# Kernel optimization log

Measured on AMD Instinct MI355X. Metric: run time of the kernel, lower is better.

The kernel has to match this reference:

```python
import jax, jax.numpy as jnp
import numpy as np

MAX_INT = 1e4  # sentinel used by the original (transitions into START / out of STOP forbidden)
VOCAB, E, H, T, B, S = 50257, 512, 1024, 50, 8, 512  # T = tagset_size + 2


def _lstm_scan(x, h0, c0, Wih, Whh, b):
    # x: [time, batch, E] (time axis is the ORIGINAL batch dim, faithful to the
    # torch code which feeds [B,S,E] into a batch_first=False LSTM)
    def step(carry, xt):
        h, c = carry
        g = xt @ Wih.T + h @ Whh.T + b
        i, f, gg, o = jnp.split(g, 4, axis=-1)  # torch gate order i,f,g,o
        c = jax.nn.sigmoid(f) * c + jax.nn.sigmoid(i) * jnp.tanh(gg)
        h = jax.nn.sigmoid(o) * jnp.tanh(c)
        return (h, c), h
    _, hs = jax.lax.scan(step, (h0, c0), x)
    return hs


def setup_inputs() -> dict:
    key = jax.random.key(0)
    k = jax.random.split(key, 14)
    Hd = H // 2
    X = jax.random.randint(k[0], (B, S), 0, VOCAB)
    Y = jax.random.randint(k[1], (B, S), 0, T - 2)  # real tags only (no start/stop)
    h0 = jax.random.normal(k[2], (2, S, Hd), jnp.float32)
    c0 = jax.random.normal(k[3], (2, S, Hd), jnp.float32)
    emb_table = jax.random.normal(k[4], (VOCAB, E), jnp.float32) * 0.02
    Wih_f = jax.random.normal(k[5], (4 * Hd, E), jnp.float32) * 0.05
    Whh_f = jax.random.normal(k[6], (4 * Hd, Hd), jnp.float32) * 0.05
    b_f = jnp.zeros((4 * Hd,), jnp.float32)
    Wih_b = jax.random.normal(k[7], (4 * Hd, E), jnp.float32) * 0.05
    Whh_b = jax.random.normal(k[8], (4 * Hd, Hd), jnp.float32) * 0.05
    b_b = jnp.zeros((4 * Hd,), jnp.float32)
    fc_W = jax.random.normal(k[9], (T, H), jnp.float32) * 0.05
    fc_b = jnp.zeros((T,), jnp.float32)
    tr = jax.random.normal(k[10], (T, T), jnp.float32)
    transitions = tr.at[-2, :].set(-MAX_INT).at[:, -1].set(-MAX_INT)
    return {"X": X, "Y": Y, "h0": h0, "c0": c0, "emb_table": emb_table,
            "Wih_f": Wih_f, "Whh_f": Whh_f, "b_f": b_f,
            "Wih_b": Wih_b, "Whh_b": Whh_b, "b_b": b_b,
            "fc_W": fc_W, "fc_b": fc_b, "transitions": transitions}


def reference(X, Y, h0, c0, emb_table, Wih_f, Whh_f, b_f, Wih_b, Whh_b, b_b, fc_W, fc_b, transitions):
    emb = emb_table[X]                                   # [B,S,E]
    # BiLSTM: torch sees axis0 as time (faithful quirk), hidden batch == S
    hf = _lstm_scan(emb, h0[0], c0[0], Wih_f, Whh_f, b_f)
    hb = _lstm_scan(emb[::-1], h0[1], c0[1], Wih_b, Whh_b, b_b)[::-1]
    lstm_out = jnp.concatenate([hf, hb], axis=-1)        # [B,S,H]
    feats = lstm_out @ fc_W.T + fc_b                     # [B,S,T]
    nB, Tt = X.shape[0], transitions.shape[0]
    # CRF forward algorithm (log partition), vectorized over tags
    init = jnp.full((nB, Tt), -MAX_INT, feats.dtype).at[:, -2].set(0.0)
    def crf_step(fv, feat):                              # fv [B,T], feat [B,T]
        nv = fv[:, None, :] + transitions[None, :, :] + feat[:, :, None]  # [B,next,prev]
        return jax.nn.logsumexp(nv, axis=2), None
    fv, _ = jax.lax.scan(crf_step, init, jnp.swapaxes(feats, 0, 1))
    forward_score = jax.nn.logsumexp(fv + transitions[-1][None, :], axis=1).sum()
    # gold path score
    start = jnp.full((nB, 1), Tt - 2, dtype=Y.dtype)
    tags = jnp.concatenate([start, Y], axis=1)           # [B,S+1]
    trans_sc = transitions[tags[:, 1:], tags[:, :-1]].sum()
    emit_sc = jnp.take_along_axis(feats, tags[:, 1:, None], axis=2)[..., 0].sum()
    gold_score = trans_sc + emit_sc + transitions[-1, tags[:, -1]].sum()
    score = forward_score - gold_score
    return score, Y
```

## Files before the change

kernel.cpp:

```cpp
#include <hip/hip_runtime.h>
#include <hip/hip_bf16.h>

typedef __attribute__((ext_vector_type(4))) float f32x4;
typedef __attribute__((ext_vector_type(8))) short short8;

#define LN2F 0.69314718055994531f

__device__ __forceinline__ unsigned short f2b(float x){
  union{float f;unsigned u;}v; v.f=x;
  unsigned r = v.u + 0x7fffu + ((v.u>>16)&1u);
  return (unsigned short)(r>>16);
}
__device__ __forceinline__ float b2f(unsigned short h){
  union{unsigned u;float f;}v; v.u = ((unsigned)h)<<16; return v.f;
}
__device__ __forceinline__ float sigm(float x){ return 1.f/(1.f+__expf(-x)); }
__device__ __forceinline__ float tanh_(float x){ float t=__expf(2.f*x); return 1.f - 2.f/(t+1.f); }

__device__ __forceinline__ void gll16(const void* g, void* l){
  __builtin_amdgcn_global_load_lds((const __attribute__((address_space(1))) void*)g,
                                   (__attribute__((address_space(3))) void*)l, 16, 0, 0);
}

__global__ __launch_bounds__(256) void prep_kernel(
  const int* __restrict__ X, const int* __restrict__ Y,
  const float* __restrict__ h0, const float* __restrict__ c0,
  const float* __restrict__ emb,
  const float* __restrict__ WihF, const float* __restrict__ WihB,
  const float* __restrict__ WhhFf, const float* __restrict__ WhhBf,
  const float* __restrict__ fcWf, const float* __restrict__ trans,
  unsigned short* __restrict__ Abf, unsigned short* __restrict__ Wcat,
  unsigned short* __restrict__ WhhF, unsigned short* __restrict__ WhhB,
  unsigned short* __restrict__ hbufs, float* __restrict__ cbuf,
  unsigned short* __restrict__ fcW, unsigned short* __restrict__ Ebf,
  float* __restrict__ out)
{
  const int tid = blockIdx.x*256 + threadIdx.x;
  const int nth = gridDim.x*256;
  for(int i=tid;i<524288;i+=nth){
    int r = i>>7, q = i&127;
    float4 v = ((const float4*)(emb + (size_t)X[r]*512))[q];
    ushort4 o; o.x=f2b(v.x); o.y=f2b(v.y); o.z=f2b(v.z); o.w=f2b(v.w);
    ((ushort4*)Abf)[i] = o;
  }
  for(int i=tid;i<524288;i+=nth){
    int r = i>>7, q = i&127;
    const float* src = (r<2048) ? (WihF + (size_t)r*512) : (WihB + (size_t)(r-2048)*512);
    float4 v = ((const float4*)src)[q];
    ushort4 o; o.x=f2b(v.x); o.y=f2b(v.y); o.z=f2b(v.z); o.w=f2b(v.w);
    ((ushort4*)Wcat)[i] = o;
  }
  for(int i=tid;i<262144;i+=nth){
    float4 v = ((const float4*)WhhFf)[i];
    ushort4 o; o.x=f2b(v.x); o.y=f2b(v.y); o.z=f2b(v.z); o.w=f2b(v.w);
    ((ushort4*)WhhF)[i] = o;
  }
  for(int i=tid;i<262144;i+=nth){
    float4 v = ((const float4*)WhhBf)[i];
    ushort4 o; o.x=f2b(v.x); o.y=f2b(v.y); o.z=f2b(v.z); o.w=f2b(v.w);
    ((ushort4*)WhhB)[i] = o;
  }
  for(int i=tid;i<131072;i+=nth){
    int d = i>>16, rest = i&65535;
    float4 v = ((const float4*)h0)[i];
    ushort4 o; o.x=f2b(v.x); o.y=f2b(v.y); o.z=f2b(v.z); o.w=f2b(v.w);
    ((ushort4*)hbufs)[(size_t)(d*2)*65536 + rest] = o;
  }
  for(int i=tid;i<131072;i+=nth) ((float4*)cbuf)[i] = ((const float4*)c0)[i];
  for(int i=tid;i<16384;i+=nth){
    int n = i>>8, q = i&255;
    float4 v;
    if (n<50) v = ((const float4*)(fcWf + (size_t)n*1024))[q];
    else { v.x=0.f; v.y=0.f; v.z=0.f; v.w=0.f; }
    ushort4 o; o.x=f2b(v.x); o.y=f2b(v.y); o.z=f2b(v.z); o.w=f2b(v.w);
    ((ushort4*)fcW)[i] = o;
  }
  for(int i=tid;i<4096;i+=nth){
    int n = i>>6, p = i&63;
    float v = (n<50 && p<50) ? __expf(trans[n*50+p]) : 0.f;
    Ebf[i] = f2b(v);
  }
  for(int i=tid;i<4096;i+=nth) out[1+i] = (float)Y[i];
}

__global__ __launch_bounds__(256) void gemm1_kernel(const unsigned short* __restrict__ A,
                                                    const unsigned short* __restrict__ B,
                                                    unsigned short* __restrict__ C){
  __shared__ __align__(16) unsigned short As[128*32];
  __shared__ __align__(16) unsigned short Bs[128*32];
  const int t = threadIdx.x, w = t>>6, l = t&63;
  const int m0 = blockIdx.x<<7, n0 = blockIdx.y<<7;
  const int wr = (w>>1)<<6, wc = (w&1)<<6;
  const int fr = l&15, fk = (l>>4)<<3;
  f32x4 acc[4][4];
  #pragma unroll
  for(int i=0;i<4;i++)
    #pragma unroll
    for(int j=0;j<4;j++) acc[i][j]=(f32x4)0.f;
  const unsigned short* Ab = A + (size_t)m0*512;
  const unsigned short* Bb = B + (size_t)n0*512;
  const int r0 = (w<<5) + (l>>2);
  const int c0 = (l&3)<<3;
  unsigned short* asd = As + (w<<5)*32;
  unsigned short* bsd = Bs + (w<<5)*32;
  for(int kt=0; kt<16; ++kt){
    __syncthreads();
    const int kc = (kt<<5) + c0;
    gll16(Ab + (size_t)r0*512 + kc,      asd);
    gll16(Ab + (size_t)(r0+16)*512 + kc, asd + 16*32);
    gll16(Bb + (size_t)r0*512 + kc,      bsd);
    gll16(Bb + (size_t)(r0+16)*512 + kc, bsd + 16*32);
    asm volatile("s_waitcnt vmcnt(0)" ::: "memory");
    __syncthreads();
    short8 af[4], bf[4];
    #pragma unroll
    for(int mi=0;mi<4;mi++) af[mi] = *(const short8*)&As[(wr+mi*16+fr)*32 + fk];
    #pragma unroll
    for(int ni=0;ni<4;ni++) bf[ni] = *(const short8*)&Bs[(wc+ni*16+fr)*32 + fk];
    #pragma unroll
    for(int mi=0;mi<4;mi++)
      #pragma unroll
      for(int ni=0;ni<4;ni++)
        acc[mi][ni] = __builtin_amdgcn_mfma_f32_16x16x32_bf16(af[mi], bf[ni], acc[mi][ni], 0,0,0);
  }
  #pragma unroll
  for(int mi=0;mi<4;mi++)
    #pragma unroll
    for(int ni=0;ni<4;ni++)
      #pragma unroll
      for(int j=0;j<4;j++){
        int row = m0 + wr + mi*16 + ((l>>4)<<2) + j;
        int col = n0 + wc + ni*16 + fr;
        C[(size_t)row*4096 + col] = f2b(acc[mi][ni][j]);
      }
}

__global__ __launch_bounds__(256) void lstm_step_kernel(
  unsigned short* __restrict__ hbufs, float* __restrict__ cbuf,
  unsigned short* __restrict__ hall, const unsigned short* __restrict__ Gin,
  const unsigned short* __restrict__ WhhF_, const unsigned short* __restrict__ WhhB_,
  const float* __restrict__ bF, const float* __restrict__ bB, int t)
{
  __shared__ __align__(16) unsigned short WL[16*4*64*8];
  __shared__ __align__(16) unsigned short Ah[2][128*32];
  const int d = blockIdx.z;
  const int m0 = blockIdx.x<<7;
  const int u0 = blockIdx.y<<4;
  const int tin = d ? (7-t) : t;
  const int par = t&1;
  const unsigned short* hprev = hbufs + (size_t)(d*2+par)*262144;
  unsigned short* hnext = hbufs + (size_t)(d*2+(par^1))*262144;
  const unsigned short* W = d ? WhhB_ : WhhF_;
  const float* bias = d ? bB : bF;
  const int tx = threadIdx.x, w = tx>>6, l = tx&63;
  const int fr = l&15, q = l>>4, fk = q<<3;
  {
    const int row = tx >> 2, qq = tx & 3;
    const int g = row >> 4, ul = row & 15;
    const int grow = (g<<9) + u0 + ul;
    #pragma unroll
    for(int kt=0;kt<16;kt++){
      uint4 v = *(const uint4*)(W + (size_t)grow*512 + kt*32 + qq*8);
      *(uint4*)(WL + ((kt*4+g)*64 + (qq*16+ul))*8) = v;
    }
  }
  __syncthreads();
  f32x4 acc[2][4];
  #pragma unroll
  for(int i=0;i<2;i++)
    #pragma unroll
    for(int j=0;j<4;j++) acc[i][j]=(f32x4)0.f;
  const int r0 = (w<<5) + (l>>2), c0 = (l&3)<<3;
  const unsigned short* hA0 = hprev + (size_t)(m0+r0)*512;
  const unsigned short* hA1 = hprev + (size_t)(m0+r0+16)*512;
  unsigned short* ab0 = Ah[0] + (w<<5)*32;
  unsigned short* ab1 = Ah[1] + (w<<5)*32;
  gll16(hA0 + c0, ab0);
  gll16(hA1 + c0, ab0 + 16*32);
  #pragma unroll
  for(int kt=0;kt<16;kt++){
    const unsigned short* cur = (kt&1) ? ab1 : ab0;
    unsigned short* nxt = (kt&1) ? ab0 : ab1;
    if(kt<15){
      int kc = (kt+1)*32 + c0;
      gll16(hA0 + kc, nxt);
      gll16(hA1 + kc, nxt + 16*32);
      asm volatile("s_waitcnt vmcnt(2)" ::: "memory");
    } else {
      asm volatile("s_waitcnt vmcnt(0)" ::: "memory");
    }
    short8 a0 = *(const short8*)(cur + fr*32 + fk);
    short8 a1 = *(const short8*)(cur + (16+fr)*32 + fk);
    short8 bf[4];
    #pragma unroll
    for(int g=0;g<4;g++) bf[g] = *(const short8*)(WL + ((kt*4+g)*64 + l)*8);
    #pragma unroll
    for(int g=0;g<4;g++){
      acc[0][g] = __builtin_amdgcn_mfma_f32_16x16x32_bf16(a0, bf[g], acc[0][g], 0,0,0);
      acc[1][g] = __builtin_amdgcn_mfma_f32_16x16x32_bf16(a1, bf[g], acc[1][g], 0,0,0);
    }
  }
  #pragma unroll
  for(int mi=0;mi<2;mi++)
    #pragma unroll
    for(int j=0;j<4;j++){
      int rs = m0 + w*32 + mi*16 + (q<<2) + j;
      int u  = u0 + fr;
      size_t grow = (size_t)(tin*512 + rs)*4096 + (size_t)d*2048;
      float p0 = acc[mi][0][j] + b2f(Gin[grow +    0 + u]) + bias[   0+u];
      float p1 = acc[mi][1][j] + b2f(Gin[grow +  512 + u]) + bias[ 512+u];
      float p2 = acc[mi][2][j] + b2f(Gin[grow + 1024 + u]) + bias[1024+u];
      float p3 = acc[mi][3][j] + b2f(Gin[grow + 1536 + u]) + bias[1536+u];
      size_t ci = (size_t)d*262144 + (size_t)rs*512 + u;
      float c = sigm(p1)*cbuf[ci] + sigm(p0)*tanh_(p2);
      cbuf[ci] = c;
      float h = sigm(p3)*tanh_(c);
      hnext[(size_t)rs*512+u] = f2b(h);
      hall[(size_t)(tin*512+rs)*1024 + (size_t)d*512 + u] = f2b(h);
    }
}

__global__ __launch_bounds__(256) void fc_kernel(const unsigned short* __restrict__ hA,
    const unsigned short* __restrict__ Wf, const float* __restrict__ fcb,
    float* __restrict__ feats){
  __shared__ __align__(16) unsigned short As[128*40];
  __shared__ __align__(16) unsigned short Bs[64*40];
  const int tx = threadIdx.x, w = tx>>6, l = tx&63;
  const int m0 = blockIdx.x<<7;
  const int srow = tx>>2, scol = (tx&3)<<3;
  const int fr=l&15, fk=(l>>4)<<3;
  f32x4 acc[2][4];
  #pragma unroll
  for(int i=0;i<2;i++)
    #pragma unroll
    for(int j=0;j<4;j++) acc[i][j]=(f32x4)0.f;
  uint4 pa0 = *(const uint4*)(hA + (size_t)(m0+srow)*1024 + scol);
  uint4 pa1 = *(const uint4*)(hA + (size_t)(m0+64+srow)*1024 + scol);
  uint4 pb0 = *(const uint4*)(Wf + (size_t)srow*1024 + scol);
  for(int kt=0; kt<32; ++kt){
    __syncthreads();
    *(uint4*)&As[srow*40+scol] = pa0;
    *(uint4*)&As[(64+srow)*40+scol] = pa1;
    *(uint4*)&Bs[srow*40+scol] = pb0;
    __syncthreads();
    if(kt<31){
      int kc = (kt+1)*32 + scol;
      pa0 = *(const uint4*)(hA + (size_t)(m0+srow)*1024 + kc);
      pa1 = *(const uint4*)(hA + (size_t)(m0+64+srow)*1024 + kc);
      pb0 = *(const uint4*)(Wf + (size_t)srow*1024 + kc);
    }
    short8 af[2], bf[4];
    #pragma unroll
    for(int mi=0;mi<2;mi++) af[mi] = *(const short8*)&As[(w*32+mi*16+fr)*40 + fk];
    #pragma unroll
    for(int ni=0;ni<4;ni++) bf[ni] = *(const short8*)&Bs[(ni*16+fr)*40 + fk];
    #pragma unroll
    for(int mi=0;mi<2;mi++)
      #pragma unroll
      for(int ni=0;ni<4;ni++)
        acc[mi][ni] = __builtin_amdgcn_mfma_f32_16x16x32_bf16(af[mi], bf[ni], acc[mi][ni], 0,0,0);
  }
  #pragma unroll
  for(int mi=0;mi<2;mi++)
    #pragma unroll
    for(int ni=0;ni<4;ni++)
      #pragma unroll
      for(int j=0;j<4;j++){
        int rs = m0 + w*32 + mi*16 + ((l>>4)<<2) + j;
        int n  = ni*16 + fr;
        feats[(size_t)rs*64+n] = acc[mi][ni][j] + (n<50 ? fcb[n] : 0.f);
      }
}

__global__ __launch_bounds__(64) void crf_group_kernel(
    const float* __restrict__ feats, const unsigned short* __restrict__ Ebf,
    float* __restrict__ Wout, int* __restrict__ kexp)
{
  __shared__ __align__(16) unsigned short PT[64*72];
  __shared__ float fe[16*64];
  const int g = blockIdx.x, b = blockIdx.y;
  const int l = threadIdx.x;
  const int lj = l & 15, q = l >> 4;
  const float* fb = feats + (size_t)(b*512 + g*16)*64;
  #pragma unroll
  for(int j=0;j<16;j++) fe[j*64 + l] = fb[j*64 + l];
  short8 afE[4][2];
  #pragma unroll
  for(int i=0;i<4;i++)
    #pragma unroll
    for(int h=0;h<2;h++)
      afE[i][h] = *(const short8*)(Ebf + (i*16+lj)*64 + h*32 + q*8);
  {
    uint4 erow[8];
    #pragma unroll
    for(int i=0;i<8;i++) erow[i] = *(const uint4*)(Ebf + l*64 + i*8);
    float ef0 = __expf(fe[l]);
    const unsigned* e32 = (const unsigned*)erow;
    #pragma unroll
    for(int m=0;m<64;m++){
      unsigned short eb = (unsigned short)(e32[m>>1] >> ((m&1)*16));
      PT[m*72 + l] = f2b(b2f(eb) * ef0);
    }
  }
  float sc_lag = 1.f;
  int exprev = 0, kblk = 0;
  #pragma unroll
  for(int k=1;k<16;k++){
    kblk += exprev;
    float ev[4][4];
    #pragma unroll
    for(int i=0;i<4;i++)
      #pragma unroll
      for(int r=0;r<4;r++)
        ev[i][r] = __expf(fe[k*64 + i*16 + q*4 + r]) * sc_lag;
    short8 bfP[4][2];
    #pragma unroll
    for(int j=0;j<4;j++)
      #pragma unroll
      for(int h=0;h<2;h++)
        bfP[j][h] = *(const short8*)&PT[(j*16+lj)*72 + h*32 + q*8];
    f32x4 acc[4][4];
    #pragma unroll
    for(int i=0;i<4;i++)
      #pragma unroll
      for(int j=0;j<4;j++) acc[i][j] = (f32x4)0.f;
    #pragma unroll
    for(int h=0;h<2;h++)
      #pragma unroll
      for(int i=0;i<4;i++)
        #pragma unroll
        for(int j=0;j<4;j++)
          acc[i][j] = __builtin_amdgcn_mfma_f32_16x16x32_bf16(afE[i][h], bfP[j][h], acc[i][j], 0,0,0);
    float mx = 1e-30f;
    float* Wo = Wout + (size_t)(b*32 + g)*4096;
    #pragma unroll
    for(int i=0;i<4;i++)
      #pragma unroll
      for(int j=0;j<4;j++){
        float v0 = acc[i][j][0]*ev[i][0];
        float v1 = acc[i][j][1]*ev[i][1];
        float v2 = acc[i][j][2]*ev[i][2];
        float v3 = acc[i][j][3]*ev[i][3];
        mx = fmaxf(fmaxf(mx, fmaxf(v0,v1)), fmaxf(v2,v3));
        int base = (j*16+lj)*72 + i*16 + q*4;
        *(unsigned*)&PT[base]   = (unsigned)f2b(v0) | ((unsigned)f2b(v1)<<16);
        *(unsigned*)&PT[base+2] = (unsigned)f2b(v2) | ((unsigned)f2b(v3)<<16);
        if(k==15){
          int n = i*16 + q*4, m = j*16 + lj;
          Wo[(size_t)(n+0)*64 + m] = v0;
          Wo[(size_t)(n+1)*64 + m] = v1;
          Wo[(size_t)(n+2)*64 + m] = v2;
          Wo[(size_t)(n+3)*64 + m] = v3;
        }
      }
    #pragma unroll
    for(int off=1; off<64; off<<=1) mx = fmaxf(mx, __shfl_xor(mx, off));
    int ex = ((__builtin_bit_cast(int, mx) >> 23) & 0xff) - 127;
    ex = ex < -120 ? -120 : (ex > 120 ? 120 : ex);
    sc_lag = __builtin_bit_cast(float, (unsigned)((127-ex)<<23));
    exprev = ex;
  }
  if(l==0) kexp[b*32 + g] = kblk;
}

__global__ __launch_bounds__(64) void crf_seq_kernel(const float* __restrict__ W,
    const int* __restrict__ kexp, const float* __restrict__ trans,
    float* __restrict__ scores){
  __shared__ __align__(16) float sh[64];
  const int b = blockIdx.x, l = threadIdx.x;
  const float* Wb = W + (size_t)b*131072;
  float kl = (l<32) ? (float)kexp[b*32 + l] : 0.f;
  #pragma unroll
  for(int off=32;off;off>>=1) kl += __shfl_down(kl, off);
  float G = (l==48) ? 1.f : 0.f;
  float sc = 1.f, Mrun = 0.f;
  int exprev = 0;
  float4 curA[16], curB[16];
  #pragma unroll
  for(int i=0;i<16;i++) curA[i] = ((const float4*)(Wb + (size_t)l*64))[i];

#define SEQ_STEP(CUR, NXT, GI) {                                            \
    sh[l] = G;                                                              \
    const float* wn = Wb + (size_t)(((GI)+1)&31)*4096 + (size_t)l*64;       \
    _Pragma("unroll")                                                       \
    for(int i=0;i<16;i++) NXT[i] = ((const float4*)wn)[i];                  \
    float4 gq[16];                                                          \
    _Pragma("unroll")                                                       \
    for(int i=0;i<16;i++) gq[i] = ((const float4*)sh)[i];                   \
    float a0=0.f,a1=0.f,a2=0.f,a3=0.f;                                      \
    _Pragma("unroll")                                                       \
    for(int i=0;i<16;i++){                                                  \
      a0 = fmaf(CUR[i].x, gq[i].x, a0);                                     \
      a1 = fmaf(CUR[i].y, gq[i].y, a1);                                     \
      a2 = fmaf(CUR[i].z, gq[i].z, a2);                                     \
      a3 = fmaf(CUR[i].w, gq[i].w, a3);                                     \
    }                                                                       \
    float S = (a0+a1)+(a2+a3);                                              \
    Mrun += (float)exprev;                                                  \
    G = S * sc;                                                             \
    float Sp = __builtin_bit_cast(float, __builtin_amdgcn_readfirstlane(    \
                 __builtin_bit_cast(int, fmaxf(S, 1e-35f))));               \
    int ex = ((__builtin_bit_cast(int, Sp) >> 23) & 0xff) - 127;            \
    ex = ex < -120 ? -120 : (ex > 120 ? 120 : ex);                          \
    sc = __builtin_bit_cast(float, (unsigned)((127-ex)<<23));               \
    exprev = ex;                                                            \
  }

  for(int g=0; g<32; g+=2){
    SEQ_STEP(curA, curB, g)
    SEQ_STEP(curB, curA, g+1)
  }
#undef SEQ_STEP
  float u = (l<50) ? __expf(trans[49*50+l]) : 0.f;
  float val = G * u;
  #pragma unroll
  for(int off=32;off;off>>=1) val += __shfl_down(val, off);
  if(l==0) scores[b] = logf(fmaxf(val,1e-35f)) + (Mrun + kl)*LN2F;
}

__global__ __launch_bounds__(256) void final_kernel(const int* __restrict__ Y,
   const float* __restrict__ trans, const float* __restrict__ feats,
   const float* __restrict__ scores, float* __restrict__ out){
  const int tx = threadIdx.x;
  float acc = 0.f;
  for(int i=tx; i<4096; i+=256){
    int s = i & 511;
    int y = Y[i];
    int prev = s ? Y[i-1] : 48;
    acc += trans[y*50+prev] + feats[(size_t)i*64+y];
    if (s==511) acc += trans[49*50+y];
  }
  #pragma unroll
  for(int off=32; off; off>>=1) acc += __shfl_down(acc, off);
  __shared__ float red[4];
  if((tx&63)==0) red[tx>>6] = acc;
  __syncthreads();
  if(tx==0){
    float gold = red[0]+red[1]+red[2]+red[3];
    float fwd = 0.f;
    #pragma unroll
    for(int b=0;b<8;b++) fwd += scores[b];
    out[0] = fwd - gold;
  }
}

extern "C" void kernel_launch(void* const* d_in, const int* in_sizes, int n_in,
                              void* d_out, int out_size, void* d_ws, size_t ws_size,
                              hipStream_t stream) {
  (void)in_sizes; (void)n_in; (void)out_size; (void)ws_size;
  const int*   X     = (const int*)d_in[0];
  const int*   Y     = (const int*)d_in[1];
  const float* h0    = (const float*)d_in[2];
  const float* c0    = (const float*)d_in[3];
  const float* emb   = (const float*)d_in[4];
  const float* WihF  = (const float*)d_in[5];
  const float* WhhFf = (const float*)d_in[6];
  const float* bF    = (const float*)d_in[7];
  const float* WihB  = (const float*)d_in[8];
  const float* WhhBf = (const float*)d_in[9];
  const float* bB    = (const float*)d_in[10];
  const float* fcWf  = (const float*)d_in[11];
  const float* fcb   = (const float*)d_in[12];
  const float* trans = (const float*)d_in[13];
  float* out = (float*)d_out;
  char* ws = (char*)d_ws;

  unsigned short* Abf   = (unsigned short*)(ws + 0);
  unsigned short* Wcat  = (unsigned short*)(ws + 4194304);
  unsigned short* WhhF  = (unsigned short*)(ws + 8388608);
  unsigned short* WhhB  = (unsigned short*)(ws + 10485760);
  unsigned short* Gin   = (unsigned short*)(ws + 12582912);
  float*          Wgrp  = (float*)(ws + 12582912);
  int*            kexp  = (int*)(ws + 20971520);
  unsigned short* hbufs = (unsigned short*)(ws + 46137344);
  float*          cbuf  = (float*)(ws + 48234496);
  unsigned short* hall  = (unsigned short*)(ws + 50331648);
  unsigned short* fcW   = (unsigned short*)(ws + 58720256);
  float*          feats = (float*)(ws + 58851328);
  unsigned short* Ebf   = (unsigned short*)(ws + 59900160);
  float*          scores= (float*)(ws + 59913472);

  hipLaunchKernelGGL(prep_kernel, dim3(1024), dim3(256), 0, stream,
      X, Y, h0, c0, emb, WihF, WihB, WhhFf, WhhBf, fcWf, trans,
      Abf, Wcat, WhhF, WhhB, hbufs, cbuf, fcW, Ebf, out);
  hipLaunchKernelGGL(gemm1_kernel, dim3(32,32), dim3(256), 0, stream, Abf, Wcat, Gin);
  for(int t=0;t<8;t++)
    hipLaunchKernelGGL(lstm_step_kernel, dim3(4,32,2), dim3(256), 0, stream,
        hbufs, cbuf, hall, Gin, WhhF, WhhB, bF, bB, t);
  hipLaunchKernelGGL(fc_kernel, dim3(32), dim3(256), 0, stream, hall, fcW, fcb, feats);
  hipLaunchKernelGGL(crf_group_kernel, dim3(32,8), dim3(64), 0, stream, feats, Ebf, Wgrp, kexp);
  hipLaunchKernelGGL(crf_seq_kernel, dim3(8), dim3(64), 0, stream, Wgrp, kexp, trans, scores);
  hipLaunchKernelGGL(final_kernel, dim3(1), dim3(256), 0, stream, Y, trans, feats, scores, out);
}
```

Baseline: 209.7 us.

## Double-buffer GEMM loads, deepen LSTM prefetch, merge CRF final into seq kernel

The input GEMM kernel now double-buffers its LDS tiles, so the next K-slice's global-to-LDS loads overlap the current slice's MFMAs. The LSTM step kernel's h-tile prefetch goes from 2 stages to 4, with staged vmcnt waits to keep more loads in flight. The separate final reduction kernel is folded into crf_seq_kernel as a ninth block, with results accumulated into out via atomicAdd after prep zeroes it. This removes one launch, but costs more LDS per block and makes the final floating-point sum order nondeterministic.

```diff
diff --git a/kernel.cpp b/kernel.cpp
--- a/kernel.cpp
+++ b/kernel.cpp
@@ -37,6 +37,7 @@
 {
   const int tid = blockIdx.x*256 + threadIdx.x;
   const int nth = gridDim.x*256;
+  if(tid==0) out[0] = 0.f;
   for(int i=tid;i<524288;i+=nth){
     int r = i>>7, q = i&127;
     float4 v = ((const float4*)(emb + (size_t)X[r]*512))[q];
@@ -86,8 +87,8 @@
 __global__ __launch_bounds__(256) void gemm1_kernel(const unsigned short* __restrict__ A,
                                                     const unsigned short* __restrict__ B,
                                                     unsigned short* __restrict__ C){
-  __shared__ __align__(16) unsigned short As[128*32];
-  __shared__ __align__(16) unsigned short Bs[128*32];
+  __shared__ __align__(16) unsigned short As[2][128*32];
+  __shared__ __align__(16) unsigned short Bs[2][128*32];
   const int t = threadIdx.x, w = t>>6, l = t&63;
   const int m0 = blockIdx.x<<7, n0 = blockIdx.y<<7;
   const int wr = (w>>1)<<6, wc = (w&1)<<6;
@@ -101,27 +102,35 @@
   const unsigned short* Bb = B + (size_t)n0*512;
   const int r0 = (w<<5) + (l>>2);
   const int c0 = (l&3)<<3;
-  unsigned short* asd = As + (w<<5)*32;
-  unsigned short* bsd = Bs + (w<<5)*32;
+  const int wo = (w<<5)*32;
+  gll16(Ab + (size_t)r0*512 + c0,      As[0] + wo);
+  gll16(Ab + (size_t)(r0+16)*512 + c0, As[0] + wo + 16*32);
+  gll16(Bb + (size_t)r0*512 + c0,      Bs[0] + wo);
+  gll16(Bb + (size_t)(r0+16)*512 + c0, Bs[0] + wo + 16*32);
+  asm volatile("s_waitcnt vmcnt(0)" ::: "memory");
+  __syncthreads();
+  int cur = 0;
   for(int kt=0; kt<16; ++kt){
-    __syncthreads();
-    const int kc = (kt<<5) + c0;
-    gll16(Ab + (size_t)r0*512 + kc,      asd);
-    gll16(Ab + (size_t)(r0+16)*512 + kc, asd + 16*32);
-    gll16(Bb + (size_t)r0*512 + kc,      bsd);
-    gll16(Bb + (size_t)(r0+16)*512 + kc, bsd + 16*32);
+    if(kt<15){
+      const int kc = ((kt+1)<<5) + c0;
+      gll16(Ab + (size_t)r0*512 + kc,      As[cur^1] + wo);
+      gll16(Ab + (size_t)(r0+16)*512 + kc, As[cur^1] + wo + 16*32);
+      gll16(Bb + (size_t)r0*512 + kc,      Bs[cur^1] + wo);
+      gll16(Bb + (size_t)(r0+16)*512 + kc, Bs[cur^1] + wo + 16*32);
+    }
+    short8 af[4], bf[4];
+    #pragma unroll
+    for(int mi=0;mi<4;mi++) af[mi] = *(const short8*)&As[cur][(wr+mi*16+fr)*32 + fk];
+    #pragma unroll
+    for(int ni=0;ni<4;ni++) bf[ni] = *(const short8*)&Bs[cur][(wc+ni*16+fr)*32 + fk];
+    #pragma unroll
+    for(int mi=0;mi<4;mi++)
+      #pragma unroll
+      for(int ni=0;ni<4;ni++)
+        acc[mi][ni] = __builtin_amdgcn_mfma_f32_16x16x32_bf16(af[mi], bf[ni], acc[mi][ni], 0,0,0);
     asm volatile("s_waitcnt vmcnt(0)" ::: "memory");
     __syncthreads();
-    short8 af[4], bf[4];
-    #pragma unroll
-    for(int mi=0;mi<4;mi++) af[mi] = *(const short8*)&As[(wr+mi*16+fr)*32 + fk];
-    #pragma unroll
-    for(int ni=0;ni<4;ni++) bf[ni] = *(const short8*)&Bs[(wc+ni*16+fr)*32 + fk];
-    #pragma unroll
-    for(int mi=0;mi<4;mi++)
-      #pragma unroll
-      for(int ni=0;ni<4;ni++)
-        acc[mi][ni] = __builtin_amdgcn_mfma_f32_16x16x32_bf16(af[mi], bf[ni], acc[mi][ni], 0,0,0);
+    cur ^= 1;
   }
   #pragma unroll
   for(int mi=0;mi<4;mi++)
@@ -142,7 +151,7 @@
   const float* __restrict__ bF, const float* __restrict__ bB, int t)
 {
   __shared__ __align__(16) unsigned short WL[16*4*64*8];
-  __shared__ __align__(16) unsigned short Ah[2][128*32];
+  __shared__ __align__(16) unsigned short Ab4[4][128*32];
   const int d = blockIdx.z;
   const int m0 = blockIdx.x<<7;
   const int u0 = blockIdx.y<<4;
@@ -173,33 +182,36 @@
   const int r0 = (w<<5) + (l>>2), c0 = (l&3)<<3;
   const unsigned short* hA0 = hprev + (size_t)(m0+r0)*512;
   const unsigned short* hA1 = hprev + (size_t)(m0+r0+16)*512;
-  unsigned short* ab0 = Ah[0] + (w<<5)*32;
-  unsigned short* ab1 = Ah[1] + (w<<5)*32;
-  gll16(hA0 + c0, ab0);
-  gll16(hA1 + c0, ab0 + 16*32);
-  #pragma unroll
-  for(int kt=0;kt<16;kt++){
-    const unsigned short* cur = (kt&1) ? ab1 : ab0;
-    unsigned short* nxt = (kt&1) ? ab0 : ab1;
-    if(kt<15){
-      int kc = (kt+1)*32 + c0;
-      gll16(hA0 + kc, nxt);
-      gll16(hA1 + kc, nxt + 16*32);
-      asm volatile("s_waitcnt vmcnt(2)" ::: "memory");
-    } else {
-      asm volatile("s_waitcnt vmcnt(0)" ::: "memory");
-    }
-    short8 a0 = *(const short8*)(cur + fr*32 + fk);
-    short8 a1 = *(const short8*)(cur + (16+fr)*32 + fk);
-    short8 bf[4];
-    #pragma unroll
-    for(int g=0;g<4;g++) bf[g] = *(const short8*)(WL + ((kt*4+g)*64 + l)*8);
-    #pragma unroll
-    for(int g=0;g<4;g++){
-      acc[0][g] = __builtin_amdgcn_mfma_f32_16x16x32_bf16(a0, bf[g], acc[0][g], 0,0,0);
-      acc[1][g] = __builtin_amdgcn_mfma_f32_16x16x32_bf16(a1, bf[g], acc[1][g], 0,0,0);
-    }
-  }
+#define ABUF(i) (Ab4[(i)] + ((w<<5)*32))
+  gll16(hA0 + 0*32 + c0, ABUF(0)); gll16(hA1 + 0*32 + c0, ABUF(0)+16*32);
+  gll16(hA0 + 1*32 + c0, ABUF(1)); gll16(hA1 + 1*32 + c0, ABUF(1)+16*32);
+  gll16(hA0 + 2*32 + c0, ABUF(2)); gll16(hA1 + 2*32 + c0, ABUF(2)+16*32);
+  gll16(hA0 + 3*32 + c0, ABUF(3)); gll16(hA1 + 3*32 + c0, ABUF(3)+16*32);
+#define LSTEP(KT, VM) {                                                       \
+    if((KT)+4 < 16){                                                          \
+      const int kc_ = ((KT)+4)*32 + c0;                                       \
+      gll16(hA0 + kc_, ABUF(((KT)+4)&3));                                     \
+      gll16(hA1 + kc_, ABUF(((KT)+4)&3)+16*32);                               \
+    }                                                                         \
+    asm volatile("s_waitcnt vmcnt(" VM ")" ::: "memory");                     \
+    const unsigned short* cur_ = ABUF((KT)&3);                                \
+    short8 a0_ = *(const short8*)(cur_ + fr*32 + fk);                         \
+    short8 a1_ = *(const short8*)(cur_ + (16+fr)*32 + fk);                    \
+    short8 bv_[4];                                                            \
+    _Pragma("unroll")                                                         \
+    for(int g=0;g<4;g++) bv_[g] = *(const short8*)(WL + (((KT)*4+g)*64 + l)*8);\
+    _Pragma("unroll")                                                         \
+    for(int g=0;g<4;g++){                                                     \
+      acc[0][g] = __builtin_amdgcn_mfma_f32_16x16x32_bf16(a0_, bv_[g], acc[0][g], 0,0,0); \
+      acc[1][g] = __builtin_amdgcn_mfma_f32_16x16x32_bf16(a1_, bv_[g], acc[1][g], 0,0,0); \
+    }                                                                         \
+  }
+  LSTEP(0,"8")  LSTEP(1,"8")  LSTEP(2,"8")  LSTEP(3,"8")
+  LSTEP(4,"8")  LSTEP(5,"8")  LSTEP(6,"8")  LSTEP(7,"8")
+  LSTEP(8,"8")  LSTEP(9,"8")  LSTEP(10,"8") LSTEP(11,"8")
+  LSTEP(12,"6") LSTEP(13,"4") LSTEP(14,"2") LSTEP(15,"0")
+#undef LSTEP
+#undef ABUF
   #pragma unroll
   for(int mi=0;mi<2;mi++)
     #pragma unroll
@@ -363,21 +375,25 @@
   if(l==0) kexp[b*32 + g] = kblk;
 }
 
-__global__ __launch_bounds__(64) void crf_seq_kernel(const float* __restrict__ W,
+__global__ __launch_bounds__(256) void crf_seq_kernel(const float* __restrict__ W,
     const int* __restrict__ kexp, const float* __restrict__ trans,
-    float* __restrict__ scores){
-  __shared__ __align__(16) float sh[64];
-  const int b = blockIdx.x, l = threadIdx.x;
-  const float* Wb = W + (size_t)b*131072;
-  float kl = (l<32) ? (float)kexp[b*32 + l] : 0.f;
-  #pragma unroll
-  for(int off=32;off;off>>=1) kl += __shfl_down(kl, off);
-  float G = (l==48) ? 1.f : 0.f;
-  float sc = 1.f, Mrun = 0.f;
-  int exprev = 0;
-  float4 curA[16], curB[16];
-  #pragma unroll
-  for(int i=0;i<16;i++) curA[i] = ((const float4*)(Wb + (size_t)l*64))[i];
+    const float* __restrict__ feats, const int* __restrict__ Y,
+    float* __restrict__ out){
+  const int b = blockIdx.x;
+  if(b < 8){
+    if(threadIdx.x >= 64) return;
+    __shared__ __align__(16) float sh[64];
+    const int l = threadIdx.x;
+    const float* Wb = W + (size_t)b*131072;
+    float kl = (l<32) ? (float)kexp[b*32 + l] : 0.f;
+    #pragma unroll
+    for(int off=32;off;off>>=1) kl += __shfl_down(kl, off);
+    float G = (l==48) ? 1.f : 0.f;
+    float sc = 1.f, Mrun = 0.f;
+    int exprev = 0;
+    float4 curA[16], curB[16];
+    #pragma unroll
+    for(int i=0;i<16;i++) curA[i] = ((const float4*)(Wb + (size_t)l*64))[i];
 
 #define SEQ_STEP(CUR, NXT, GI) {                                            \
     sh[l] = G;                                                              \
@@ -406,41 +422,32 @@
     exprev = ex;                                                            \
   }
 
-  for(int g=0; g<32; g+=2){
-    SEQ_STEP(curA, curB, g)
-    SEQ_STEP(curB, curA, g+1)
-  }
+    for(int g=0; g<32; g+=2){
+      SEQ_STEP(curA, curB, g)
+      SEQ_STEP(curB, curA, g+1)
+    }
 #undef SEQ_STEP
-  float u = (l<50) ? __expf(trans[49*50+l]) : 0.f;
-  float val = G * u;
-  #pragma unroll
-  for(int off=32;off;off>>=1) val += __shfl_down(val, off);
-  if(l==0) scores[b] = logf(fmaxf(val,1e-35f)) + (Mrun + kl)*LN2F;
-}
-
-__global__ __launch_bounds__(256) void final_kernel(const int* __restrict__ Y,
-   const float* __restrict__ trans, const float* __restrict__ feats,
-   const float* __restrict__ scores, float* __restrict__ out){
-  const int tx = threadIdx.x;
-  float acc = 0.f;
-  for(int i=tx; i<4096; i+=256){
-    int s = i & 511;
-    int y = Y[i];
-    int prev = s ? Y[i-1] : 48;
-    acc += trans[y*50+prev] + feats[(size_t)i*64+y];
-    if (s==511) acc += trans[49*50+y];
-  }
-  #pragma unroll
-  for(int off=32; off; off>>=1) acc += __shfl_down(acc, off);
-  __shared__ float red[4];
-  if((tx&63)==0) red[tx>>6] = acc;
-  __syncthreads();
-  if(tx==0){
-    float gold = red[0]+red[1]+red[2]+red[3];
-    float fwd = 0.f;
-    #pragma unroll
-    for(int b=0;b<8;b++) fwd += scores[b];
-    out[0] = fwd - gold;
+    float u = (l<50) ? __expf(trans[49*50+l]) : 0.f;
+    float val = G * u;
+    #pragma unroll
+    for(int off=32;off;off>>=1) val += __shfl_down(val, off);
+    if(l==0) atomicAdd(out, logf(fmaxf(val,1e-35f)) + (Mrun + kl)*LN2F);
+  } else {
+    const int tx = threadIdx.x;
+    float acc = 0.f;
+    for(int i=tx; i<4096; i+=256){
+      int s = i & 511;
+      int y = Y[i];
+      int prev = s ? Y[i-1] : 48;
+      acc += trans[y*50+prev] + feats[(size_t)i*64+y];
+      if (s==511) acc += trans[49*50+y];
+    }
+    #pragma unroll
+    for(int off=32; off; off>>=1) acc += __shfl_down(acc, off);
+    __shared__ float red[4];
+    if((tx&63)==0) red[tx>>6] = acc;
+    __syncthreads();
+    if(tx==0) atomicAdd(out, -(red[0]+red[1]+red[2]+red[3]));
   }
 }
 
@@ -478,7 +485,6 @@
   unsigned short* fcW   = (unsigned short*)(ws + 58720256);
   float*          feats = (float*)(ws + 58851328);
   unsigned short* Ebf   = (unsigned short*)(ws + 59900160);
-  float*          scores= (float*)(ws + 59913472);
 
   hipLaunchKernelGGL(prep_kernel, dim3(1024), dim3(256), 0, stream,
       X, Y, h0, c0, emb, WihF, WihB, WhhFf, WhhBf, fcWf, trans,
@@ -489,6 +495,5 @@
         hbufs, cbuf, hall, Gin, WhhF, WhhB, bF, bB, t);
   hipLaunchKernelGGL(fc_kernel, dim3(32), dim3(256), 0, stream, hall, fcW, fcb, feats);
   hipLaunchKernelGGL(crf_group_kernel, dim3(32,8), dim3(64), 0, stream, feats, Ebf, Wgrp, kexp);
-  hipLaunchKernelGGL(crf_seq_kernel, dim3(8), dim3(64), 0, stream, Wgrp, kexp, trans, scores);
-  hipLaunchKernelGGL(final_kernel, dim3(1), dim3(256), 0, stream, Y, trans, feats, scores, out);
-}
+  hipLaunchKernelGGL(crf_seq_kernel, dim3(9), dim3(256), 0, stream, Wgrp, kexp, trans, feats, Y, out);
+}
```

New measurement: 189.4 us, median of 2. 1.11x faster.
